# Kernel optimization log

Measured on AMD Instinct MI355X. Metric: run time of the kernel, lower is better.

Reference implementation:

```python
import jax, jax.numpy as jnp
import numpy as np

B, S, E, H = 8, 1025, 1408, 16
D = E // H  # 88 head_dim


def setup_inputs() -> dict:
    key = jax.random.key(0)
    ks = jax.random.split(key, 12)
    w_scale = 0.02
    hidden_states = jax.random.normal(ks[0], (B, S, E), dtype=jnp.float32)
    ang = jax.random.uniform(ks[1], (S, D // 2), dtype=jnp.float32) * (2.0 * np.pi)
    freqs_cos = jnp.cos(ang)
    freqs_sin = jnp.sin(ang)
    Wq = jax.random.normal(ks[2], (E, E), dtype=jnp.float32) * w_scale
    bq = jax.random.normal(ks[3], (E,), dtype=jnp.float32) * w_scale
    Wk = jax.random.normal(ks[4], (E, E), dtype=jnp.float32) * w_scale
    bk = jax.random.normal(ks[5], (E,), dtype=jnp.float32) * w_scale
    Wv = jax.random.normal(ks[6], (E, E), dtype=jnp.float32) * w_scale
    bv = jax.random.normal(ks[7], (E,), dtype=jnp.float32) * w_scale
    Wo = jax.random.normal(ks[8], (E, E), dtype=jnp.float32) * w_scale
    bo = jax.random.normal(ks[9], (E,), dtype=jnp.float32) * w_scale
    return {"hidden_states": hidden_states, "freqs_cos": freqs_cos, "freqs_sin": freqs_sin,
            "Wq": Wq, "bq": bq, "Wk": Wk, "bk": bk, "Wv": Wv, "bv": bv, "Wo": Wo, "bo": bo}


def _apply_rope(x, cos, sin):
    # x: (B,S,H,D); interpret last dim as D/2 complex pairs (real, imag)
    xr = x[..., 0::2]  # (B,S,H,D/2) -- pairs laid out interleaved after reshape(..., -1, 2)
    xi = x[..., 1::2]
    c = cos[None, :, None, :]  # (1,S,1,D/2)
    s = sin[None, :, None, :]
    or_ = xr * c - xi * s
    oi_ = xr * s + xi * c
    # interleave back: (..., D/2, 2) -> (..., D)
    return jnp.stack([or_, oi_], axis=-1).reshape(x.shape)


def reference(hidden_states, freqs_cos, freqs_sin, Wq, bq, Wk, bk, Wv, bv, Wo, bo):
    b, s, e = hidden_states.shape
    h, d = H, D
    q = (hidden_states @ Wq.T + bq).reshape(b, s, h, d)
    k = (hidden_states @ Wk.T + bk).reshape(b, s, h, d)
    v = (hidden_states @ Wv.T + bv).reshape(b, s, h, d)
    q = _apply_rope(q, freqs_cos, freqs_sin)
    k = _apply_rope(k, freqs_cos, freqs_sin)
    scale = d ** (-0.5)
    # (B,H,S,S) attention scores; no mask, non-causal, dropout=0 (eval)
    scores = jnp.einsum("bshd,bthd->bhst", q, k) * scale
    w = jax.nn.softmax(scores, axis=-1)
    out = jnp.einsum("bhst,bthd->bshd", w, v).reshape(b, s, e)
    return out @ Wo.T + bo
```

## Files before the change

kernel.cpp:

```cpp
#include <hip/hip_runtime.h>
#include <stdint.h>
#include <stddef.h>

#define Bsz 8
#define Ssz 1025
#define Esz 1408
#define Hsz 16
#define Dsz 88
#define Msz (Bsz * Ssz)
#define HALF_E (Esz / 2)
#define HALF_D (Dsz / 2)
#define SPAD 1088
#define QSC 0.15379182f

typedef __attribute__((ext_vector_type(8))) short short8;
typedef __attribute__((ext_vector_type(4))) float f32x4;

__device__ __forceinline__ unsigned short f2bf(float f) {
  union { float f; unsigned u; } v; v.f = f;
  unsigned r = v.u + 0x7fffu + ((v.u >> 16) & 1u);
  return (unsigned short)(r >> 16);
}
__device__ __forceinline__ unsigned fbits(float f) {
  union { float f; unsigned u; } v; v.f = f; return v.u;
}
__device__ __forceinline__ float fexp2(float x) {
#if __has_builtin(__builtin_amdgcn_exp2f)
  return __builtin_amdgcn_exp2f(x);
#else
  return __expf(x * 0.6931471805599453f);
#endif
}

__global__ void cast_kernel(const float* __restrict__ in, unsigned short* __restrict__ out, int n4) {
  int i = blockIdx.x * blockDim.x + threadIdx.x;
  if (i >= n4) return;
  float4 v = ((const float4*)in)[i];
  uint2 o;
  o.x = (unsigned)f2bf(v.x) | ((unsigned)f2bf(v.y) << 16);
  o.y = (unsigned)f2bf(v.z) | ((unsigned)f2bf(v.w) << 16);
  ((uint2*)out)[i] = o;
}

template <int OUT_BF16>
__global__ __launch_bounds__(256)
void gemm_bt(const unsigned short* __restrict__ A, const unsigned short* __restrict__ Bw,
             const float* __restrict__ bias, void* __restrict__ Cout,
             int M, int N, int K) {
  __shared__ __attribute__((aligned(16))) unsigned short sA[128 * 32];
  __shared__ __attribute__((aligned(16))) unsigned short sB[128 * 32];
  const int tid  = threadIdx.x;
  const int wave = tid >> 6;
  const int lane = tid & 63;
  const int m0 = blockIdx.y * 128;
  const int n0 = blockIdx.x * 128;
  const int wm = (wave >> 1) * 64;
  const int wn = (wave & 1) * 64;
  const int l15 = lane & 15;
  const int q8  = (lane >> 4) * 8;
  const int lr  = lane >> 2;
  const int lc  = (lane & 3) * 8;

  const f32x4 z4 = {0.f, 0.f, 0.f, 0.f};
  f32x4 acc[4][4];
  for (int i = 0; i < 4; i++)
    for (int j = 0; j < 4; j++) acc[i][j] = z4;

  for (int k0 = 0; k0 < K; k0 += 32) {
    __syncthreads();
#pragma unroll
    for (int c = 0; c < 2; c++) {
      int row = wave * 32 + c * 16;
      int gm = m0 + row + lr; if (gm > M - 1) gm = M - 1;
      const unsigned short* gpa = A + (size_t)gm * K + (k0 + lc);
      __builtin_amdgcn_global_load_lds(
          (__attribute__((address_space(1))) void*)gpa,
          (__attribute__((address_space(3))) void*)(&sA[row * 32]),
          16, 0, 0);
      int gn = n0 + row + lr;
      const unsigned short* gpb = Bw + (size_t)gn * K + (k0 + lc);
      __builtin_amdgcn_global_load_lds(
          (__attribute__((address_space(1))) void*)gpb,
          (__attribute__((address_space(3))) void*)(&sB[row * 32]),
          16, 0, 0);
    }
    __syncthreads();

    short8 af[4], bfv[4];
#pragma unroll
    for (int i = 0; i < 4; i++) af[i]  = *(const short8*)&sA[(wm + i * 16 + l15) * 32 + q8];
#pragma unroll
    for (int j = 0; j < 4; j++) bfv[j] = *(const short8*)&sB[(wn + j * 16 + l15) * 32 + q8];
#pragma unroll
    for (int i = 0; i < 4; i++)
#pragma unroll
      for (int j = 0; j < 4; j++)
        acc[i][j] = __builtin_amdgcn_mfma_f32_16x16x32_bf16(af[i], bfv[j], acc[i][j], 0, 0, 0);
  }

#pragma unroll
  for (int i = 0; i < 4; i++) {
#pragma unroll
    for (int j = 0; j < 4; j++) {
      int n = n0 + wn + j * 16 + l15;
      float bias_n = bias[n];
#pragma unroll
      for (int r = 0; r < 4; r++) {
        int m = m0 + wm + i * 16 + (lane >> 4) * 4 + r;
        if (m < M) {
          float val = acc[i][j][r] + bias_n;
          if (OUT_BF16) ((unsigned short*)Cout)[(size_t)m * N + n] = f2bf(val);
          else          ((float*)Cout)[(size_t)m * N + n] = val;
        }
      }
    }
  }
}

__global__ __launch_bounds__(256)
void gemm_qkv(const unsigned short* __restrict__ A, const unsigned short* __restrict__ W,
              const float* __restrict__ bq, const float* __restrict__ bk,
              const float* __restrict__ bv,
              const float* __restrict__ cosp, const float* __restrict__ sinp,
              unsigned short* __restrict__ qkv, int M, int K) {
  __shared__ __attribute__((aligned(16))) unsigned short sA[128 * 32];
  __shared__ __attribute__((aligned(16))) unsigned short sB[128 * 32];
  const int tid  = threadIdx.x;
  const int wave = tid >> 6;
  const int lane = tid & 63;
  const int m0 = blockIdx.y * 128;
  const int n0 = blockIdx.x * 128;
  const int wm = (wave >> 1) * 64;
  const int wn = (wave & 1) * 64;
  const int l15 = lane & 15;
  const int q8  = (lane >> 4) * 8;
  const int quad4 = (lane >> 4) * 4;
  const int lr  = lane >> 2;
  const int lc  = (lane & 3) * 8;

  const f32x4 z4 = {0.f, 0.f, 0.f, 0.f};
  f32x4 acc[4][4];
  for (int i = 0; i < 4; i++)
    for (int j = 0; j < 4; j++) acc[i][j] = z4;

  for (int k0 = 0; k0 < K; k0 += 32) {
    __syncthreads();
#pragma unroll
    for (int c = 0; c < 2; c++) {
      int row = wave * 32 + c * 16;
      int gm = m0 + row + lr; if (gm > M - 1) gm = M - 1;
      const unsigned short* gpa = A + (size_t)gm * K + (k0 + lc);
      __builtin_amdgcn_global_load_lds(
          (__attribute__((address_space(1))) void*)gpa,
          (__attribute__((address_space(3))) void*)(&sA[row * 32]),
          16, 0, 0);
      int gn = n0 + row + lr;
      const unsigned short* gpb = W + (size_t)gn * K + (k0 + lc);
      __builtin_amdgcn_global_load_lds(
          (__attribute__((address_space(1))) void*)gpb,
          (__attribute__((address_space(3))) void*)(&sB[row * 32]),
          16, 0, 0);
    }
    __syncthreads();

    short8 af[4], bfv[4];
#pragma unroll
    for (int i = 0; i < 4; i++) af[i]  = *(const short8*)&sA[(wm + i * 16 + l15) * 32 + q8];
#pragma unroll
    for (int j = 0; j < 4; j++) bfv[j] = *(const short8*)&sB[(wn + j * 16 + l15) * 32 + q8];
#pragma unroll
    for (int i = 0; i < 4; i++)
#pragma unroll
      for (int j = 0; j < 4; j++)
        acc[i][j] = __builtin_amdgcn_mfma_f32_16x16x32_bf16(af[i], bfv[j], acc[i][j], 0, 0, 0);
  }

  const int sel   = blockIdx.x / 11;
  const int nloc0 = (blockIdx.x % 11) * 128;
  const float* bias = (sel == 0) ? bq : (sel == 1) ? bk : bv;
  unsigned short* outb = qkv + (size_t)sel * ((size_t)Msz * Esz);

#pragma unroll
  for (int i = 0; i < 4; i++) {
#pragma unroll
    for (int j = 0; j < 4; j++) {
      int nl = nloc0 + wn + j * 16 + l15;
      float bias_n = bias[nl];
      int dd = nl % Dsz;
      int jrot = dd >> 1;
      bool isEven = (nl & 1) == 0;
#pragma unroll
      for (int r = 0; r < 4; r++) {
        int m = m0 + wm + i * 16 + quad4 + r;
        float val = acc[i][j][r] + bias_n;
        if (sel < 2) {
          float pv = __shfl_xor(val, 1, 64);
          int sp = m - (m / Ssz) * Ssz;
          float c  = cosp[sp * HALF_D + jrot];
          float sn = sinp[sp * HALF_D + jrot];
          val = isEven ? (val * c - pv * sn) : (pv * sn + val * c);
        }
        if (sel == 0) val *= QSC;
        if (m < M) outb[(size_t)m * Esz + nl] = f2bf(val);
      }
    }
  }
}

__global__ __launch_bounds__(256)
void vtrans_kernel(const unsigned short* __restrict__ vb, unsigned short* __restrict__ vt) {
  __shared__ unsigned short sT[64 * 89 + 8];
  const int tid = threadIdx.x;
  const int st = blockIdx.x, hh = blockIdx.y, bb = blockIdx.z;
  const short8 z8 = {0, 0, 0, 0, 0, 0, 0, 0};
  const unsigned short* src = vb + (size_t)(bb * Ssz) * Esz + hh * Dsz;
#pragma unroll
  for (int it = 0; it < 3; it++) {
    int g = it * 256 + tid;
    if (g < 704) {
      int r = g / 11, gc = g - r * 11;
      int s = st * 64 + r;
      short8 v = z8;
      if (s < Ssz) v = *(const short8*)(src + (size_t)s * Esz + gc * 8);
#pragma unroll
      for (int i = 0; i < 8; i++) sT[r * 89 + gc * 8 + i] = v[i];
    }
  }
  __syncthreads();
  unsigned short* dst = vt + (size_t)((bb * Hsz + hh) * Dsz) * SPAD + st * 64;
#pragma unroll
  for (int it = 0; it < 3; it++) {
    int g = it * 256 + tid;
    if (g < 704) {
      int d = g >> 3, sc = g & 7;
      short8 v;
#pragma unroll
      for (int i = 0; i < 8; i++) v[i] = sT[(sc * 8 + i) * 89 + d];
      *(short8*)(dst + (size_t)d * SPAD + sc * 8) = v;
    }
  }
}

__global__ __launch_bounds__(256)
void attn_kernel(const unsigned short* __restrict__ qp, const unsigned short* __restrict__ kp,
                 const unsigned short* __restrict__ vt, unsigned short* __restrict__ op) {
  __shared__ __attribute__((aligned(16))) unsigned short sK[64 * 88 + 16];
  __shared__ __attribute__((aligned(16))) unsigned short sVT[96 * 72];
  __shared__ __attribute__((aligned(16))) unsigned short sP[64 * 72];
  const int tid  = threadIdx.x;
  const int wave = tid >> 6, lane = tid & 63;
  const int qt = blockIdx.x, hh = blockIdx.y, bb = blockIdx.z;
  const int l15 = lane & 15, quad = lane >> 4;
  const int quad4 = quad * 4;
  const short8 z8 = {0, 0, 0, 0, 0, 0, 0, 0};

  short8 qf[3];
  {
    int s = qt * 64 + wave * 16 + l15; if (s > Ssz - 1) s = Ssz - 1;
    const unsigned short* qrow = qp + (size_t)(bb * Ssz + s) * Esz + hh * Dsz;
#pragma unroll
    for (int ks = 0; ks < 3; ks++) {
      short8 v = z8;
      if (!(ks == 2 && quad == 3)) v = *(const short8*)(qrow + ks * 32 + quad * 8);
      qf[ks] = v;
    }
  }

  const unsigned short* kbase  = kp + (size_t)(bb * Ssz) * Esz + hh * Dsz;
  const unsigned short* vtbase = vt + (size_t)((bb * Hsz + hh) * Dsz) * SPAD;
  unsigned* sPu = (unsigned*)sP;

  float m_i = -1e30f, l_i = 0.f;
  const f32x4 z4 = {0.f, 0.f, 0.f, 0.f};
  f32x4 o_acc[6];
#pragma unroll
  for (int jd = 0; jd < 6; jd++) o_acc[jd] = z4;

  for (int kt = 0; kt < 17; kt++) {
    __syncthreads();
    for (int c = wave; c < 11; c += 4) {
      int g = c * 64 + lane;
      int r = g / 11, gc = g - r * 11;
      int t = kt * 64 + r; if (t > Ssz - 1) t = Ssz - 1;
      const unsigned short* srcp = kbase + (size_t)t * Esz + gc * 8;
      __builtin_amdgcn_global_load_lds(
          (__attribute__((address_space(1))) void*)srcp,
          (__attribute__((address_space(3))) void*)(&sK[c * 512]),
          16, 0, 0);
    }
#pragma unroll
    for (int it = 0; it < 3; it++) {
      int g = it * 256 + tid;
      if (g < 704) {
        int d = g >> 3, sc2 = g & 7;
        short8 v = *(const short8*)(vtbase + (size_t)d * SPAD + kt * 64 + sc2 * 8);
        *(short8*)&sVT[d * 72 + sc2 * 8] = v;
      }
    }
    __syncthreads();

    f32x4 st[4];
#pragma unroll
    for (int j = 0; j < 4; j++) st[j] = z4;
#pragma unroll
    for (int ks = 0; ks < 3; ks++) {
#pragma unroll
      for (int j = 0; j < 4; j++) {
        short8 bk8 = *(const short8*)&sK[(j * 16 + l15) * 88 + ks * 32 + quad * 8];
        st[j] = __builtin_amdgcn_mfma_f32_16x16x32_bf16(bk8, qf[ks], st[j], 0, 0, 0);
      }
    }

    if (kt == 16) {
#pragma unroll
      for (int j = 0; j < 4; j++)
#pragma unroll
        for (int r = 0; r < 4; r++)
          if (j != 0 || r != 0) st[j][r] = -1e30f;
      if (quad != 0) st[0][0] = -1e30f;
    }

    float rmax = st[0][0];
#pragma unroll
    for (int j = 0; j < 4; j++)
#pragma unroll
      for (int r = 0; r < 4; r++) rmax = fmaxf(rmax, st[j][r]);
    rmax = fmaxf(rmax, __shfl_xor(rmax, 16, 64));
    rmax = fmaxf(rmax, __shfl_xor(rmax, 32, 64));

    float mnew = fmaxf(m_i, rmax);
    float alpha = fexp2(m_i - mnew);
    m_i = mnew;

    float rsum = 0.f;
#pragma unroll
    for (int j = 0; j < 4; j++) {
      float p0 = fexp2(st[j][0] - mnew);
      float p1 = fexp2(st[j][1] - mnew);
      float p2 = fexp2(st[j][2] - mnew);
      float p3 = fexp2(st[j][3] - mnew);
      rsum += (p0 + p1) + (p2 + p3);
      unsigned w0 = __builtin_amdgcn_perm(fbits(p1) + 0x8000u, fbits(p0) + 0x8000u, 0x07060302u);
      unsigned w1 = __builtin_amdgcn_perm(fbits(p3) + 0x8000u, fbits(p2) + 0x8000u, 0x07060302u);
      int base = (wave * 16 + l15) * 36 + j * 8 + quad * 2;
      sPu[base]     = w0;
      sPu[base + 1] = w1;
    }
    rsum += __shfl_xor(rsum, 16, 64);
    rsum += __shfl_xor(rsum, 32, 64);
    l_i = l_i * alpha + rsum;

    float ar[4];
#pragma unroll
    for (int r = 0; r < 4; r++) ar[r] = __shfl(alpha, quad4 + r, 64);
#pragma unroll
    for (int jd = 0; jd < 6; jd++)
#pragma unroll
      for (int r = 0; r < 4; r++) o_acc[jd][r] *= ar[r];

#pragma unroll
    for (int ks2 = 0; ks2 < 2; ks2++) {
      short8 ap = *(const short8*)&sP[(wave * 16 + l15) * 72 + ks2 * 32 + quad * 8];
#pragma unroll
      for (int jd = 0; jd < 6; jd++) {
        short8 bv8 = *(const short8*)&sVT[(jd * 16 + l15) * 72 + ks2 * 32 + quad * 8];
        o_acc[jd] = __builtin_amdgcn_mfma_f32_16x16x32_bf16(ap, bv8, o_acc[jd], 0, 0, 0);
      }
    }
  }

  float lr4[4];
#pragma unroll
  for (int r = 0; r < 4; r++) lr4[r] = __shfl(l_i, quad4 + r, 64);
#pragma unroll
  for (int jd = 0; jd < 6; jd++) {
    int d = jd * 16 + l15;
#pragma unroll
    for (int r = 0; r < 4; r++) {
      int s = qt * 64 + wave * 16 + quad4 + r;
      if (s < Ssz && d < Dsz) {
        float val = o_acc[jd][r] / lr4[r];
        op[((size_t)(bb * Ssz + s)) * Esz + hh * Dsz + d] = f2bf(val);
      }
    }
  }
}

extern "C" void kernel_launch(void* const* d_in, const int* in_sizes, int n_in,
                              void* d_out, int out_size, void* d_ws, size_t ws_size,
                              hipStream_t stream) {
  const float* hs = (const float*)d_in[0];
  const float* fc = (const float*)d_in[1];
  const float* fs = (const float*)d_in[2];
  const float* Wq = (const float*)d_in[3];
  const float* bq = (const float*)d_in[4];
  const float* Wk = (const float*)d_in[5];
  const float* bk = (const float*)d_in[6];
  const float* Wv = (const float*)d_in[7];
  const float* bv = (const float*)d_in[8];
  const float* Wo = (const float*)d_in[9];
  const float* bo = (const float*)d_in[10];
  float* out = (float*)d_out;

  const size_t ME = (size_t)Msz * Esz;
  const size_t EE = (size_t)Esz * Esz;
  unsigned short* hsb = (unsigned short*)d_ws;
  unsigned short* wqb = hsb + ME;
  unsigned short* wkb = wqb + EE;
  unsigned short* wvb = wkb + EE;
  unsigned short* qb  = wvb + EE;
  unsigned short* kb  = qb  + ME;
  unsigned short* vb  = kb  + ME;
  unsigned short* wob = vb  + ME;
  unsigned short* vtb = hsb;
  unsigned short* aob = vb;

  int nh4 = (int)(ME / 4);
  int nw4 = (int)(EE / 4);
  cast_kernel<<<(nh4 + 255) / 256, 256, 0, stream>>>(hs, hsb, nh4);
  cast_kernel<<<(nw4 + 255) / 256, 256, 0, stream>>>(Wq, wqb, nw4);
  cast_kernel<<<(nw4 + 255) / 256, 256, 0, stream>>>(Wk, wkb, nw4);
  cast_kernel<<<(nw4 + 255) / 256, 256, 0, stream>>>(Wv, wvb, nw4);
  cast_kernel<<<(nw4 + 255) / 256, 256, 0, stream>>>(Wo, wob, nw4);

  dim3 gq(33, (Msz + 127) / 128);
  gemm_qkv<<<gq, 256, 0, stream>>>(hsb, wqb, bq, bk, bv, fc, fs, qb, Msz, Esz);

  vtrans_kernel<<<dim3(17, Hsz, Bsz), 256, 0, stream>>>(vb, vtb);

  attn_kernel<<<dim3(17, Hsz, Bsz), 256, 0, stream>>>(qb, kb, vtb, aob);

  dim3 gg(Esz / 128, (Msz + 127) / 128);
  gemm_bt<0><<<gg, 256, 0, stream>>>(aob, wob, bo, out, Msz, Esz, Esz);
}
```

Before: 540.0 us.

## Process two query tiles per attention block and merge weight casts

Each attention block now handles 128 query rows (two 64-row subtiles) against each K/V tile loaded into LDS, halving the K/V global loads and shared-memory staging per query. The grid shrinks from 17 to 9 query tiles per head. The four weight-cast launches are also merged into one kernel, with the workspace reordered so the weights sit contiguously. Keeping double accumulators raises register pressure and may lower occupancy, and the smaller grid reduces parallelism.

```diff
diff --git a/kernel.cpp b/kernel.cpp
--- a/kernel.cpp
+++ b/kernel.cpp
@@ -40,6 +40,20 @@
   o.x = (unsigned)f2bf(v.x) | ((unsigned)f2bf(v.y) << 16);
   o.y = (unsigned)f2bf(v.z) | ((unsigned)f2bf(v.w) << 16);
   ((uint2*)out)[i] = o;
+}
+
+__global__ void cast4_kernel(const float* __restrict__ a, const float* __restrict__ b,
+                             const float* __restrict__ c, const float* __restrict__ d,
+                             unsigned short* __restrict__ out, int n4each) {
+  int i = blockIdx.x * blockDim.x + threadIdx.x;
+  if (i >= 4 * n4each) return;
+  int sel = i / n4each, off = i - sel * n4each;
+  const float* src = (sel == 0) ? a : (sel == 1) ? b : (sel == 2) ? c : d;
+  float4 v = ((const float4*)src)[off];
+  uint2 o;
+  o.x = (unsigned)f2bf(v.x) | ((unsigned)f2bf(v.y) << 16);
+  o.y = (unsigned)f2bf(v.z) | ((unsigned)f2bf(v.w) << 16);
+  ((uint2*)(out))[i] = o;
 }
 
 template <int OUT_BF16>
@@ -254,15 +268,16 @@
   const int quad4 = quad * 4;
   const short8 z8 = {0, 0, 0, 0, 0, 0, 0, 0};
 
-  short8 qf[3];
-  {
-    int s = qt * 64 + wave * 16 + l15; if (s > Ssz - 1) s = Ssz - 1;
+  short8 qf[2][3];
+#pragma unroll
+  for (int st2 = 0; st2 < 2; st2++) {
+    int s = qt * 128 + st2 * 64 + wave * 16 + l15; if (s > Ssz - 1) s = Ssz - 1;
     const unsigned short* qrow = qp + (size_t)(bb * Ssz + s) * Esz + hh * Dsz;
 #pragma unroll
     for (int ks = 0; ks < 3; ks++) {
       short8 v = z8;
       if (!(ks == 2 && quad == 3)) v = *(const short8*)(qrow + ks * 32 + quad * 8);
-      qf[ks] = v;
+      qf[st2][ks] = v;
     }
   }
 
@@ -270,11 +285,13 @@
   const unsigned short* vtbase = vt + (size_t)((bb * Hsz + hh) * Dsz) * SPAD;
   unsigned* sPu = (unsigned*)sP;
 
-  float m_i = -1e30f, l_i = 0.f;
+  float m_i[2] = {-1e30f, -1e30f}, l_i[2] = {0.f, 0.f};
   const f32x4 z4 = {0.f, 0.f, 0.f, 0.f};
-  f32x4 o_acc[6];
-#pragma unroll
-  for (int jd = 0; jd < 6; jd++) o_acc[jd] = z4;
+  f32x4 o_acc[2][6];
+#pragma unroll
+  for (int st2 = 0; st2 < 2; st2++)
+#pragma unroll
+    for (int jd = 0; jd < 6; jd++) o_acc[st2][jd] = z4;
 
   for (int kt = 0; kt < 17; kt++) {
     __syncthreads();
@@ -299,88 +316,94 @@
     }
     __syncthreads();
 
-    f32x4 st[4];
-#pragma unroll
-    for (int j = 0; j < 4; j++) st[j] = z4;
-#pragma unroll
-    for (int ks = 0; ks < 3; ks++) {
+#pragma unroll
+    for (int st2 = 0; st2 < 2; st2++) {
+      f32x4 stv[4];
+#pragma unroll
+      for (int j = 0; j < 4; j++) stv[j] = z4;
+#pragma unroll
+      for (int ks = 0; ks < 3; ks++) {
+#pragma unroll
+        for (int j = 0; j < 4; j++) {
+          short8 bk8 = *(const short8*)&sK[(j * 16 + l15) * 88 + ks * 32 + quad * 8];
+          stv[j] = __builtin_amdgcn_mfma_f32_16x16x32_bf16(bk8, qf[st2][ks], stv[j], 0, 0, 0);
+        }
+      }
+
+      if (kt == 16) {
+#pragma unroll
+        for (int j = 0; j < 4; j++)
+#pragma unroll
+          for (int r = 0; r < 4; r++)
+            if (j != 0 || r != 0) stv[j][r] = -1e30f;
+        if (quad != 0) stv[0][0] = -1e30f;
+      }
+
+      float rmax = stv[0][0];
+#pragma unroll
+      for (int j = 0; j < 4; j++)
+#pragma unroll
+        for (int r = 0; r < 4; r++) rmax = fmaxf(rmax, stv[j][r]);
+      rmax = fmaxf(rmax, __shfl_xor(rmax, 16, 64));
+      rmax = fmaxf(rmax, __shfl_xor(rmax, 32, 64));
+
+      float mnew = fmaxf(m_i[st2], rmax);
+      float alpha = fexp2(m_i[st2] - mnew);
+      m_i[st2] = mnew;
+
+      float rsum = 0.f;
 #pragma unroll
       for (int j = 0; j < 4; j++) {
-        short8 bk8 = *(const short8*)&sK[(j * 16 + l15) * 88 + ks * 32 + quad * 8];
-        st[j] = __builtin_amdgcn_mfma_f32_16x16x32_bf16(bk8, qf[ks], st[j], 0, 0, 0);
-      }
-    }
-
-    if (kt == 16) {
-#pragma unroll
-      for (int j = 0; j < 4; j++)
-#pragma unroll
-        for (int r = 0; r < 4; r++)
-          if (j != 0 || r != 0) st[j][r] = -1e30f;
-      if (quad != 0) st[0][0] = -1e30f;
-    }
-
-    float rmax = st[0][0];
-#pragma unroll
-    for (int j = 0; j < 4; j++)
-#pragma unroll
-      for (int r = 0; r < 4; r++) rmax = fmaxf(rmax, st[j][r]);
-    rmax = fmaxf(rmax, __shfl_xor(rmax, 16, 64));
-    rmax = fmaxf(rmax, __shfl_xor(rmax, 32, 64));
-
-    float mnew = fmaxf(m_i, rmax);
-    float alpha = fexp2(m_i - mnew);
-    m_i = mnew;
-
-    float rsum = 0.f;
-#pragma unroll
-    for (int j = 0; j < 4; j++) {
-      float p0 = fexp2(st[j][0] - mnew);
-      float p1 = fexp2(st[j][1] - mnew);
-      float p2 = fexp2(st[j][2] - mnew);
-      float p3 = fexp2(st[j][3] - mnew);
-      rsum += (p0 + p1) + (p2 + p3);
-      unsigned w0 = __builtin_amdgcn_perm(fbits(p1) + 0x8000u, fbits(p0) + 0x8000u, 0x07060302u);
-      unsigned w1 = __builtin_amdgcn_perm(fbits(p3) + 0x8000u, fbits(p2) + 0x8000u, 0x07060302u);
-      int base = (wave * 16 + l15) * 36 + j * 8 + quad * 2;
-      sPu[base]     = w0;
-      sPu[base + 1] = w1;
-    }
-    rsum += __shfl_xor(rsum, 16, 64);
-    rsum += __shfl_xor(rsum, 32, 64);
-    l_i = l_i * alpha + rsum;
-
-    float ar[4];
-#pragma unroll
-    for (int r = 0; r < 4; r++) ar[r] = __shfl(alpha, quad4 + r, 64);
-#pragma unroll
-    for (int jd = 0; jd < 6; jd++)
-#pragma unroll
-      for (int r = 0; r < 4; r++) o_acc[jd][r] *= ar[r];
-
-#pragma unroll
-    for (int ks2 = 0; ks2 < 2; ks2++) {
-      short8 ap = *(const short8*)&sP[(wave * 16 + l15) * 72 + ks2 * 32 + quad * 8];
-#pragma unroll
-      for (int jd = 0; jd < 6; jd++) {
-        short8 bv8 = *(const short8*)&sVT[(jd * 16 + l15) * 72 + ks2 * 32 + quad * 8];
-        o_acc[jd] = __builtin_amdgcn_mfma_f32_16x16x32_bf16(ap, bv8, o_acc[jd], 0, 0, 0);
-      }
-    }
-  }
-
-  float lr4[4];
-#pragma unroll
-  for (int r = 0; r < 4; r++) lr4[r] = __shfl(l_i, quad4 + r, 64);
-#pragma unroll
-  for (int jd = 0; jd < 6; jd++) {
-    int d = jd * 16 + l15;
-#pragma unroll
-    for (int r = 0; r < 4; r++) {
-      int s = qt * 64 + wave * 16 + quad4 + r;
-      if (s < Ssz && d < Dsz) {
-        float val = o_acc[jd][r] / lr4[r];
-        op[((size_t)(bb * Ssz + s)) * Esz + hh * Dsz + d] = f2bf(val);
+        float p0 = fexp2(stv[j][0] - mnew);
+        float p1 = fexp2(stv[j][1] - mnew);
+        float p2 = fexp2(stv[j][2] - mnew);
+        float p3 = fexp2(stv[j][3] - mnew);
+        rsum += (p0 + p1) + (p2 + p3);
+        unsigned w0 = __builtin_amdgcn_perm(fbits(p1) + 0x8000u, fbits(p0) + 0x8000u, 0x07060302u);
+        unsigned w1 = __builtin_amdgcn_perm(fbits(p3) + 0x8000u, fbits(p2) + 0x8000u, 0x07060302u);
+        int base = (wave * 16 + l15) * 36 + j * 8 + quad * 2;
+        sPu[base]     = w0;
+        sPu[base + 1] = w1;
+      }
+      rsum += __shfl_xor(rsum, 16, 64);
+      rsum += __shfl_xor(rsum, 32, 64);
+      l_i[st2] = l_i[st2] * alpha + rsum;
+
+      float ar[4];
+#pragma unroll
+      for (int r = 0; r < 4; r++) ar[r] = __shfl(alpha, quad4 + r, 64);
+#pragma unroll
+      for (int jd = 0; jd < 6; jd++)
+#pragma unroll
+        for (int r = 0; r < 4; r++) o_acc[st2][jd][r] *= ar[r];
+
+#pragma unroll
+      for (int ks2 = 0; ks2 < 2; ks2++) {
+        short8 ap = *(const short8*)&sP[(wave * 16 + l15) * 72 + ks2 * 32 + quad * 8];
+#pragma unroll
+        for (int jd = 0; jd < 6; jd++) {
+          short8 bv8 = *(const short8*)&sVT[(jd * 16 + l15) * 72 + ks2 * 32 + quad * 8];
+          o_acc[st2][jd] = __builtin_amdgcn_mfma_f32_16x16x32_bf16(ap, bv8, o_acc[st2][jd], 0, 0, 0);
+        }
+      }
+    }
+  }
+
+#pragma unroll
+  for (int st2 = 0; st2 < 2; st2++) {
+    float lr4[4];
+#pragma unroll
+    for (int r = 0; r < 4; r++) lr4[r] = __shfl(l_i[st2], quad4 + r, 64);
+#pragma unroll
+    for (int jd = 0; jd < 6; jd++) {
+      int d = jd * 16 + l15;
+#pragma unroll
+      for (int r = 0; r < 4; r++) {
+        int s = qt * 128 + st2 * 64 + wave * 16 + quad4 + r;
+        if (s < Ssz && d < Dsz) {
+          float val = o_acc[st2][jd][r] / lr4[r];
+          op[((size_t)(bb * Ssz + s)) * Esz + hh * Dsz + d] = f2bf(val);
+        }
       }
     }
   }
@@ -408,27 +431,24 @@
   unsigned short* wqb = hsb + ME;
   unsigned short* wkb = wqb + EE;
   unsigned short* wvb = wkb + EE;
-  unsigned short* qb  = wvb + EE;
+  unsigned short* wob = wvb + EE;
+  unsigned short* qb  = wob + EE;
   unsigned short* kb  = qb  + ME;
   unsigned short* vb  = kb  + ME;
-  unsigned short* wob = vb  + ME;
   unsigned short* vtb = hsb;
   unsigned short* aob = vb;
 
   int nh4 = (int)(ME / 4);
   int nw4 = (int)(EE / 4);
   cast_kernel<<<(nh4 + 255) / 256, 256, 0, stream>>>(hs, hsb, nh4);
-  cast_kernel<<<(nw4 + 255) / 256, 256, 0, stream>>>(Wq, wqb, nw4);
-  cast_kernel<<<(nw4 + 255) / 256, 256, 0, stream>>>(Wk, wkb, nw4);
-  cast_kernel<<<(nw4 + 255) / 256, 256, 0, stream>>>(Wv, wvb, nw4);
-  cast_kernel<<<(nw4 + 255) / 256, 256, 0, stream>>>(Wo, wob, nw4);
+  cast4_kernel<<<(4 * nw4 + 255) / 256, 256, 0, stream>>>(Wq, Wk, Wv, Wo, wqb, nw4);
 
   dim3 gq(33, (Msz + 127) / 128);
   gemm_qkv<<<gq, 256, 0, stream>>>(hsb, wqb, bq, bk, bv, fc, fs, qb, Msz, Esz);
 
   vtrans_kernel<<<dim3(17, Hsz, Bsz), 256, 0, stream>>>(vb, vtb);
 
-  attn_kernel<<<dim3(17, Hsz, Bsz), 256, 0, stream>>>(qb, kb, vtb, aob);
+  attn_kernel<<<dim3(9, Hsz, Bsz), 256, 0, stream>>>(qb, kb, vtb, aob);
 
   dim3 gg(Esz / 128, (Msz + 127) / 128);
   gemm_bt<0><<<gg, 256, 0, stream>>>(aob, wob, bo, out, Msz, Esz, Esz);
```

Result: slower. 580.4 us (+7.5%).
